# Kernel tuning notes

Hardware: AMD Instinct MI355X
Metric: run time of the kernel (lower is better)

The kernel has to match this reference:

```python
import jax, jax.numpy as jnp
import numpy as np
import math

B, R, C = 4, 512, 512
E, H, D, M, F = 256, 16, 16, 16, 512  # embed, heads, qkv_dim, ms_hidden, ff_hidden
EPS = 1e-5


def setup_inputs() -> dict:
    key = jax.random.key(0)
    ks = jax.random.split(key, 20)
    s = lambda fan_in: 1.0 / math.sqrt(fan_in)
    u = lambda k, shape, lim: jax.random.uniform(k, shape, jnp.float32, -lim, lim)
    mix1_init = (1 / 2) ** 0.5
    mix2_init = (1 / 16) ** 0.5
    return {
        "row_emb": jax.random.normal(ks[0], (B, R, E), jnp.float32),
        "col_emb": jax.random.normal(ks[1], (B, C, E), jnp.float32),
        "cost_mat": jax.random.uniform(ks[2], (B, R, C), jnp.float32),
        "Wq": u(ks[3], (E, H * D), s(E)),
        "Wk": u(ks[4], (E, H * D), s(E)),
        "Wv": u(ks[5], (E, H * D), s(E)),
        "mix1_w": u(ks[6], (H, 2, M), mix1_init),
        "mix1_b": u(ks[7], (H, M), mix1_init),
        "mix2_w": u(ks[8], (H, M, 1), mix2_init),
        "mix2_b": u(ks[9], (H, 1), mix2_init),
        "Wc": u(ks[10], (H * D, E), s(H * D)),
        "bc": u(ks[11], (E,), s(H * D)),
        "W1": u(ks[12], (E, F), s(E)),
        "b1": u(ks[13], (F,), s(E)),
        "W2": u(ks[14], (F, E), s(F)),
        "b2": u(ks[15], (E,), s(F)),
        "g1": jnp.ones((E,), jnp.float32),
        "be1": jnp.zeros((E,), jnp.float32),
        "g2": jnp.ones((E,), jnp.float32),
        "be2": jnp.zeros((E,), jnp.float32),
    }


def _instance_norm(x, gamma, beta):
    # InstanceNorm1d on x permuted to (B, E, L): normalize over seq dim per (b, channel)
    mean = jnp.mean(x, axis=1, keepdims=True)          # [B,1,E]
    var = jnp.mean((x - mean) ** 2, axis=1, keepdims=True)
    return (x - mean) * jax.lax.rsqrt(var + EPS) * gamma + beta


def reference(row_emb, col_emb, cost_mat, Wq, Wk, Wv, mix1_w, mix1_b, mix2_w,
              mix2_b, Wc, bc, W1, b1, W2, b2, g1, be1, g2, be2):
    # QKV projections, split heads: [B,L,H*D] -> [B,H,L,D]
    q = (row_emb @ Wq).reshape(B, R, H, D).transpose(0, 2, 1, 3)
    k = (col_emb @ Wk).reshape(B, C, H, D).transpose(0, 2, 1, 3)
    v = (col_emb @ Wv).reshape(B, C, H, D).transpose(0, 2, 1, 3)

    dot = jnp.einsum('bhrd,bhcd->bhrc', q, k) / math.sqrt(D)
    cost = jnp.broadcast_to(cost_mat[:, None, :, :], (B, H, R, C))
    two = jnp.stack((dot, cost), axis=-1)               # [B,H,R,C,2]

    # per-head 2 -> M -> 1 mixing MLP over scores
    ms1 = jnp.einsum('bhrcs,hsm->bhrcm', two, mix1_w) + mix1_b[None, :, None, None, :]
    ms1 = jax.nn.relu(ms1)
    mixed = jnp.einsum('bhrcm,hm->bhrc', ms1, mix2_w[:, :, 0]) + mix2_b[:, 0][None, :, None, None]

    weights = jax.nn.softmax(mixed, axis=-1)            # [B,H,R,C]
    out = jnp.einsum('bhrc,bhcd->bhrd', weights, v)
    out_concat = out.transpose(0, 2, 1, 3).reshape(B, R, H * D)

    mh = out_concat @ Wc + bc                           # multi_head_combine

    # TransformerFFN with instance norm
    x = _instance_norm(row_emb + mh, g1, be1)
    ffn = jax.nn.relu(x @ W1 + b1) @ W2 + b2
    return _instance_norm(x + ffn, g2, be2)
```

## Files before the change

kernel.cpp:

```cpp
#include <hip/hip_runtime.h>
#include <hip/hip_bf16.h>

typedef __hip_bfloat16 bf16;
typedef __hip_bfloat162 bf162;
typedef _Float16 f16;
typedef __attribute__((ext_vector_type(2))) _Float16 h2;
typedef __attribute__((ext_vector_type(4))) _Float16 f16x4;
typedef __attribute__((ext_vector_type(8))) short short8;
typedef __attribute__((ext_vector_type(4))) short short4v;
typedef __attribute__((ext_vector_type(4))) float f32x4;

#define B_ 4
#define R_ 512
#define C_ 512
#define E_ 256
#define H_ 16
#define D_ 16

__device__ __forceinline__ float b2f(bf16 x) { return __bfloat162float(x); }
__device__ __forceinline__ void stout(bf16* p, float v) { *p = __float2bfloat16(v); }
__device__ __forceinline__ void stout(f16* p, float v) { *p = (f16)v; }

__global__ __launch_bounds__(256) void transpose_cvt_kernel(
    const float* __restrict__ Wq, const float* __restrict__ Wk, const float* __restrict__ Wv,
    const float* __restrict__ Wc, const float* __restrict__ W1, const float* __restrict__ W2,
    bf16* __restrict__ WqT, bf16* __restrict__ WkT, bf16* __restrict__ WvT,
    bf16* __restrict__ WcT, bf16* __restrict__ W1T, bf16* __restrict__ W2T,
    float* __restrict__ statsZ)
{
    __shared__ bf16 tile[32][33];
    const int wsel = blockIdx.y;
    const int tx = blockIdx.x;
    if (wsel == 0 && tx >= 64) {
        const int idx = (tx - 64) * 256 + threadIdx.x;
        if (idx < 4096) statsZ[idx] = 0.f;
        return;
    }
    const float* src; bf16* dst; int K, N; float scl = 1.0f;
    switch (wsel) {
        case 0: src = Wq; dst = WqT; K = 256; N = 256; scl = 0.25f; break;
        case 1: src = Wk; dst = WkT; K = 256; N = 256; break;
        case 2: src = Wv; dst = WvT; K = 256; N = 256; break;
        case 3: src = Wc; dst = WcT; K = 256; N = 256; break;
        case 4: src = W1; dst = W1T; K = 256; N = 512; break;
        default: src = W2; dst = W2T; K = 512; N = 256; break;
    }
    const int ntiles = (K >> 5) * (N >> 5);
    if (tx >= ntiles) return;
    const int ncnt = N >> 5;
    const int tk = tx / ncnt, tn = tx % ncnt;
    const int c = threadIdx.x & 31, r = threadIdx.x >> 5;
#pragma unroll
    for (int i = 0; i < 4; i++)
        tile[r + i * 8][c] = __float2bfloat16(scl * src[(size_t)(tk * 32 + r + i * 8) * N + tn * 32 + c]);
    __syncthreads();
#pragma unroll
    for (int i = 0; i < 4; i++)
        dst[(size_t)(tn * 32 + r + i * 8) * K + tk * 32 + c] = tile[c][r + i * 8];
}

template <int AMODE, typename OT, int BM, int BN, bool BIAS, int RES, bool RELU, bool STATS>
__device__ __forceinline__ void mfma_gemm_body(
    const void* __restrict__ Ap, const bf16* __restrict__ BT,
    const float* __restrict__ bias, const void* __restrict__ Res,
    const float* __restrict__ normS, const float* __restrict__ normG, const float* __restrict__ normB,
    float* __restrict__ statsOut, OT* __restrict__ Cout,
    int M, int N, int K, int bx, int by)
{
    constexpr int MT = BM / 32, NT = BN / 32;
    constexpr int AEL = BM * 64 / 256, BEL = BN * 64 / 256;
    __shared__ __align__(16) bf16 As[BM * 80];
    __shared__ __align__(16) bf16 Bs[BN * 80];
    const int tid = threadIdx.x;
    const int wid = tid >> 6, lane = tid & 63;
    const int wm = wid >> 1, wn = wid & 1;
    const int fr = lane & 15, quad = lane >> 4;
    const int m0 = by * BM, n0 = bx * BN;
    const int arow = (AEL == 16) ? (tid >> 2) : (tid >> 3);
    const int akg  = (AEL == 16) ? ((tid & 3) << 4) : ((tid & 7) << 3);
    const int brow = (BEL == 16) ? (tid >> 2) : (tid >> 3);
    const int bkg  = (BEL == 16) ? ((tid & 3) << 4) : ((tid & 7) << 3);

    f32x4 acc[MT][NT];
#pragma unroll
    for (int mt = 0; mt < MT; mt++)
#pragma unroll
        for (int nt = 0; nt < NT; nt++) acc[mt][nt] = (f32x4){0.f, 0.f, 0.f, 0.f};

    for (int k0 = 0; k0 < K; k0 += 64) {
        if constexpr (AMODE == 0) {
            const short8* gp = (const short8*)((const bf16*)Ap + (size_t)(m0 + arow) * K + k0 + akg);
#pragma unroll
            for (int t8 = 0; t8 < AEL / 8; t8++) *(short8*)(&As[arow * 80 + akg + 8 * t8]) = gp[t8];
        } else if constexpr (AMODE == 1) {
            const float4* gp = (const float4*)((const float*)Ap + (size_t)(m0 + arow) * K + k0 + akg);
#pragma unroll
            for (int j = 0; j < AEL / 4; j++) {
                const float4 f = gp[j];
                *(bf162*)(&As[arow * 80 + akg + j * 4])     = __float22bfloat162_rn(make_float2(f.x, f.y));
                *(bf162*)(&As[arow * 80 + akg + j * 4 + 2]) = __float22bfloat162_rn(make_float2(f.z, f.w));
            }
        } else {
            const int bb = (m0 + arow) >> 9;
            const bf16* ap = (const bf16*)Ap + (size_t)(m0 + arow) * K + k0 + akg;
            bf16 tmp[AEL];
#pragma unroll
            for (int t8 = 0; t8 < AEL / 8; t8++) *(short8*)(tmp + 8 * t8) = ((const short8*)ap)[t8];
#pragma unroll
            for (int j = 0; j < AEL; j++) {
                const int e = k0 + akg + j;
                const float s = normS[bb * 256 + e], sq = normS[1024 + bb * 256 + e];
                const float mn = s * (1.f / 512.f);
                float var = sq * (1.f / 512.f) - mn * mn; var = fmaxf(var, 0.f);
                As[arow * 80 + akg + j] = __float2bfloat16(
                    (b2f(tmp[j]) - mn) * rsqrtf(var + 1e-5f) * normG[e] + normB[e]);
            }
        }
        {
            const short8* gp = (const short8*)(BT + (size_t)(n0 + brow) * K + k0 + bkg);
#pragma unroll
            for (int t8 = 0; t8 < BEL / 8; t8++) *(short8*)(&Bs[brow * 80 + bkg + 8 * t8]) = gp[t8];
        }
        __syncthreads();

        short8 af[MT][2], bfr[NT][2];
#pragma unroll
        for (int mt = 0; mt < MT; mt++) {
            const int ar = wm * (BM / 2) + mt * 16 + fr;
#pragma unroll
            for (int kh = 0; kh < 2; kh++)
                af[mt][kh] = *(const short8*)(&As[ar * 80 + quad * 8 + kh * 32]);
        }
#pragma unroll
        for (int nt = 0; nt < NT; nt++) {
            const int br = wn * (BN / 2) + nt * 16 + fr;
#pragma unroll
            for (int kh = 0; kh < 2; kh++)
                bfr[nt][kh] = *(const short8*)(&Bs[br * 80 + quad * 8 + kh * 32]);
        }
#pragma unroll
        for (int kh = 0; kh < 2; kh++)
#pragma unroll
            for (int mt = 0; mt < MT; mt++)
#pragma unroll
                for (int nt = 0; nt < NT; nt++)
                    acc[mt][nt] = __builtin_amdgcn_mfma_f32_16x16x32_bf16(
                        af[mt][kh], bfr[nt][kh], acc[mt][nt], 0, 0, 0);
        __syncthreads();
    }

    float vsum[NT], vss[NT];
#pragma unroll
    for (int nt = 0; nt < NT; nt++) { vsum[nt] = 0.f; vss[nt] = 0.f; }
#pragma unroll
    for (int mt = 0; mt < MT; mt++) {
#pragma unroll
        for (int nt = 0; nt < NT; nt++) {
#pragma unroll
            for (int i = 0; i < 4; i++) {
                const int row = m0 + wm * (BM / 2) + mt * 16 + quad * 4 + i;
                const int col = n0 + wn * (BN / 2) + nt * 16 + fr;
                float v = acc[mt][nt][i];
                if (BIAS) v += bias[col];
                if constexpr (RES == 1) v += ((const float*)Res)[(size_t)row * N + col];
                if constexpr (RES == 3) {
                    const int bb = row >> 9;
                    const float yv = b2f(((const bf16*)Res)[(size_t)row * N + col]);
                    const float s = normS[bb * 256 + col], sq = normS[1024 + bb * 256 + col];
                    const float mn = s * (1.f / 512.f);
                    float var = sq * (1.f / 512.f) - mn * mn; var = fmaxf(var, 0.f);
                    v += (yv - mn) * rsqrtf(var + 1e-5f) * normG[col] + normB[col];
                }
                if (RELU) v = fmaxf(v, 0.f);
                stout(&Cout[(size_t)row * N + col], v);
                if (STATS) { vsum[nt] += v; vss[nt] += v * v; }
            }
        }
    }
    if constexpr (STATS) {
        float* sred = (float*)As;
#pragma unroll
        for (int nt = 0; nt < NT; nt++) {
            float a = vsum[nt]; a += __shfl_xor(a, 16, 64); a += __shfl_xor(a, 32, 64);
            float c = vss[nt];  c += __shfl_xor(c, 16, 64); c += __shfl_xor(c, 32, 64);
            if (quad == 0) {
                const int cl = wn * (BN / 2) + nt * 16 + fr;
                sred[wm * (2 * BN) + cl * 2 + 0] = a;
                sred[wm * (2 * BN) + cl * 2 + 1] = c;
            }
        }
        __syncthreads();
        if (tid < 2 * BN) {
            const int cl = tid >> 1, w = tid & 1;
            const float tot = sred[cl * 2 + w] + sred[2 * BN + cl * 2 + w];
            atomicAdd(&statsOut[w * 1024 + (m0 >> 9) * 256 + n0 + cl], tot);
        }
    }
}

template <int AMODE, typename OT, int BM, int BN, bool BIAS, int RES, bool RELU, bool STATS>
__global__ __launch_bounds__(256) void mfma_gemm_kernel(
    const void* __restrict__ Ap, const bf16* __restrict__ BT,
    const float* __restrict__ bias, const void* __restrict__ Res,
    const float* __restrict__ normS, const float* __restrict__ normG, const float* __restrict__ normB,
    float* __restrict__ statsOut, OT* __restrict__ Cout, int M, int N, int K)
{
    mfma_gemm_body<AMODE, OT, BM, BN, BIAS, RES, RELU, STATS>(
        Ap, BT, bias, Res, normS, normG, normB, statsOut, Cout,
        M, N, K, blockIdx.x, blockIdx.y);
}

__global__ __launch_bounds__(256) void qkv_kernel(
    const float* __restrict__ rowE, const float* __restrict__ colE,
    const bf16* __restrict__ WqT, const bf16* __restrict__ WkT, const bf16* __restrict__ WvT,
    f16* __restrict__ qo, f16* __restrict__ ko, f16* __restrict__ vo)
{
    const int z = blockIdx.z;
    const float* A = (z == 0) ? rowE : colE;
    const bf16* BT = (z == 0) ? WqT : (z == 1) ? WkT : WvT;
    f16* out = (z == 0) ? qo : (z == 1) ? ko : vo;
    mfma_gemm_body<1, f16, 32, 64, false, 0, false, false>(
        A, BT, nullptr, nullptr, nullptr, nullptr, nullptr, nullptr, out,
        2048, 256, 256, blockIdx.x, blockIdx.y);
}

__global__ __launch_bounds__(256) void attn_kernel(
    const f16* __restrict__ q, const f16* __restrict__ k, const f16* __restrict__ v,
    const float* __restrict__ cost, const float* __restrict__ m1w, const float* __restrict__ m1b,
    const float* __restrict__ m2w, const float* __restrict__ m2b,
    bf16* __restrict__ sa)
{
    __shared__ __align__(16) short kbuf[512 * 16];
    __shared__ __align__(16) _Float16 vbufT[16 * 520];

    const int rt = blockIdx.x, h = blockIdx.y, b = blockIdx.z;
    const int tid = threadIdx.x, wid = tid >> 6, lane = tid & 63;
    const int quad = lane >> 4, fr = lane & 15;
    const int row_m = rt * 64 + wid * 16 + fr;

    const f16x4 qf = *(const f16x4*)(q + (size_t)(b * R_ + row_m) * 256 + h * 16 + (quad << 2));

    {
        const int lc0 = tid >> 1, dp = (tid & 1) * 8;
        const size_t gbase = (size_t)(b * C_) * 256 + h * 16 + dp;
#pragma unroll
        for (int it = 0; it < 4; it++) {
            const int lc = it * 128 + lc0;
            const size_t g = gbase + (size_t)lc * 256;
            *(short8*)(&kbuf[lc * 16 + (dp ^ ((lc & 1) << 3))]) = *(const short8*)(k + g);
            const short8 vv = *(const short8*)(v + g);
#pragma unroll
            for (int u = 0; u < 8; u++) vbufT[(dp + u) * 520 + lc] = ((const _Float16*)&vv)[u];
        }
    }

    h2 w1a2[8], w1b2[8], b1h[8], w2p[8];
#pragma unroll
    for (int i = 0; i < 8; i++) {
        h2 t;
        t.x = (f16)m1w[h * 32 + 2 * i];      t.y = (f16)m1w[h * 32 + 2 * i + 1];      w1a2[i] = t;
        t.x = (f16)m1w[h * 32 + 16 + 2 * i]; t.y = (f16)m1w[h * 32 + 17 + 2 * i];     w1b2[i] = t;
        t.x = (f16)m1b[h * 16 + 2 * i];      t.y = (f16)m1b[h * 16 + 2 * i + 1];      b1h[i] = t;
        t.x = (f16)m2w[h * 16 + 2 * i];      t.y = (f16)m2w[h * 16 + 2 * i + 1];      w2p[i] = t;
    }
    const float b2v = m2b[h];
    const h2 zero2 = (h2)(f16)0;

    const float* crow = cost + (size_t)(b * R_ + row_m) * C_;
    float4 cf[2][8];
#pragma unroll
    for (int t = 0; t < 8; t++) cf[0][t] = *(const float4*)(crow + t * 16 + (quad << 2));

    __syncthreads();

    f32x4 oaccT = (f32x4){0.f, 0.f, 0.f, 0.f};
    float lsum = 0.f, m_run = -3.0e30f;

#pragma unroll
    for (int cs = 0; cs < 4; cs++) {
        if (cs < 3) {
#pragma unroll
            for (int t = 0; t < 8; t++)
                cf[(cs + 1) & 1][t] = *(const float4*)(crow + (cs + 1) * 128 + t * 16 + (quad << 2));
        }
        f32x4 sc[8];
#pragma unroll
        for (int t = 0; t < 8; t++) {
            const int c = cs * 128 + t * 16 + fr;
            const f16x4 kf = *(const f16x4*)(&kbuf[c * 16 + ((quad << 2) ^ ((fr & 1) << 3))]);
            sc[t] = __builtin_amdgcn_mfma_f32_16x16x16f16(kf, qf, (f32x4){0.f, 0.f, 0.f, 0.f}, 0, 0, 0);
        }
#pragma unroll
        for (int t = 0; t < 8; t++) {
            const float4 cq = cf[cs & 1][t];
            const float carr[4] = {cq.x, cq.y, cq.z, cq.w};
#pragma unroll
            for (int i = 0; i < 4; i++) {
                const f16 doth = (f16)sc[t][i], csth = (f16)carr[i];
                h2 dot2; dot2.x = doth; dot2.y = doth;
                h2 cst2; cst2.x = csth; cst2.y = csth;
                h2 acc2 = zero2;
#pragma unroll
                for (int mm = 0; mm < 8; mm++) {
                    h2 tt = dot2 * w1a2[mm] + b1h[mm];
                    tt = cst2 * w1b2[mm] + tt;
                    tt = __builtin_elementwise_max(tt, zero2);
                    acc2 = tt * w2p[mm] + acc2;
                }
                sc[t][i] = b2v + (float)acc2.x + (float)acc2.y;
            }
        }
        float mx = fmaxf(fmaxf(sc[0][0], sc[0][1]), fmaxf(sc[0][2], sc[0][3]));
#pragma unroll
        for (int t = 1; t < 8; t++)
            mx = fmaxf(mx, fmaxf(fmaxf(sc[t][0], sc[t][1]), fmaxf(sc[t][2], sc[t][3])));
        mx = fmaxf(mx, __shfl_xor(mx, 16, 64));
        mx = fmaxf(mx, __shfl_xor(mx, 32, 64));
        const float mnew = fmaxf(m_run, mx);
        const float fac = __expf(m_run - mnew);
        m_run = mnew;
        lsum *= fac;
        oaccT[0] *= fac; oaccT[1] *= fac; oaccT[2] *= fac; oaccT[3] *= fac;

#pragma unroll
        for (int p = 0; p < 8; p++) {
            f16x4 pf;
#pragma unroll
            for (int j = 0; j < 4; j++) {
                const float e = __expf(sc[p][j] - m_run);
                lsum += e;
                pf[j] = (f16)e;
            }
            const f16x4 vf = *(const f16x4*)(&vbufT[fr * 520 + cs * 128 + p * 16 + (quad << 2)]);
            oaccT = __builtin_amdgcn_mfma_f32_16x16x16f16(vf, pf, oaccT, 0, 0, 0);
        }
    }

    lsum += __shfl_xor(lsum, 16, 64);
    lsum += __shfl_xor(lsum, 32, 64);
    const float inv = 1.f / lsum;
    short4v o;
#pragma unroll
    for (int i = 0; i < 4; i++) o[i] = __builtin_bit_cast(short, __float2bfloat16(oaccT[i] * inv));
    *(short4v*)((short*)sa + (size_t)(b * R_ + row_m) * 256 + h * 16 + (quad << 2)) = o;
}

__global__ __launch_bounds__(256) void apply_in2_kernel(
    const bf16* __restrict__ xin, const float* __restrict__ stats,
    const float* __restrict__ g, const float* __restrict__ be, float* __restrict__ outp)
{
    const int base = (blockIdx.x * 256 + threadIdx.x) * 4;
    const int b = base >> 17;
    const bf162* xp = (const bf162*)(xin + base);
    const float2 x0 = __bfloat1622float2(xp[0]), x1 = __bfloat1622float2(xp[1]);
    const float xv[4] = {x0.x, x0.y, x1.x, x1.y};
    float4 rr;
    float* rp = (float*)&rr;
#pragma unroll
    for (int j = 0; j < 4; j++) {
        const int e = (base & 255) + j;
        const float s = stats[b * 256 + e], sq = stats[1024 + b * 256 + e];
        const float mn = s * (1.f / 512.f);
        float var = sq * (1.f / 512.f) - mn * mn; var = fmaxf(var, 0.f);
        rp[j] = (xv[j] - mn) * rsqrtf(var + 1e-5f) * g[e] + be[e];
    }
    *(float4*)(outp + base) = rr;
}

extern "C" void kernel_launch(void* const* d_in, const int* in_sizes, int n_in,
                              void* d_out, int out_size, void* d_ws, size_t ws_size,
                              hipStream_t stream)
{
    (void)in_sizes; (void)n_in; (void)out_size; (void)ws_size;
    const float* row_emb = (const float*)d_in[0];
    const float* col_emb = (const float*)d_in[1];
    const float* cost    = (const float*)d_in[2];
    const float* Wq  = (const float*)d_in[3];
    const float* Wk  = (const float*)d_in[4];
    const float* Wv  = (const float*)d_in[5];
    const float* m1w = (const float*)d_in[6];
    const float* m1b = (const float*)d_in[7];
    const float* m2w = (const float*)d_in[8];
    const float* m2b = (const float*)d_in[9];
    const float* Wc  = (const float*)d_in[10];
    const float* bc  = (const float*)d_in[11];
    const float* W1  = (const float*)d_in[12];
    const float* b1  = (const float*)d_in[13];
    const float* W2  = (const float*)d_in[14];
    const float* b2  = (const float*)d_in[15];
    const float* g1  = (const float*)d_in[16];
    const float* be1 = (const float*)d_in[17];
    const float* g2  = (const float*)d_in[18];
    const float* be2 = (const float*)d_in[19];
    float* out = (float*)d_out;

    char* w = (char*)d_ws;
    const size_t MB = 1u << 20;
    f16*  sq  = (f16*)(w + 0 * MB);
    f16*  sk  = (f16*)(w + 1 * MB);
    f16*  sv  = (f16*)(w + 2 * MB);
    bf16* sa  = (bf16*)(w + 3 * MB);
    bf16* sy  = (bf16*)(w + 4 * MB);
    bf16* st  = (bf16*)(w + 5 * MB);
    bf16* shm = (bf16*)(w + 6 * MB);
    bf16* WqT = (bf16*)(w + 8 * MB);
    bf16* WkT = WqT + 65536;
    bf16* WvT = WkT + 65536;
    bf16* WcT = WvT + 65536;
    bf16* W1T = WcT + 65536;
    bf16* W2T = W1T + 131072;
    float* stats1 = (float*)(w + 9 * MB);
    float* stats2 = stats1 + 2048;

    const dim3 blk(256);

    transpose_cvt_kernel<<<dim3(128, 6), blk, 0, stream>>>(
        Wq, Wk, Wv, Wc, W1, W2, WqT, WkT, WvT, WcT, W1T, W2T, stats1);

    qkv_kernel<<<dim3(4, 64, 3), blk, 0, stream>>>(row_emb, col_emb, WqT, WkT, WvT, sq, sk, sv);

    attn_kernel<<<dim3(8, 16, 4), blk, 0, stream>>>(
        sq, sk, sv, cost, m1w, m1b, m2w, m2b, sa);

    mfma_gemm_kernel<0, bf16, 32, 32, true, 1, false, true><<<dim3(8, 64), blk, 0, stream>>>(
        sa, WcT, bc, row_emb, nullptr, nullptr, nullptr, stats1, sy, 2048, 256, 256);

    mfma_gemm_kernel<2, bf16, 32, 64, true, 0, true, false><<<dim3(8, 64), blk, 0, stream>>>(
        sy, W1T, b1, nullptr, stats1, g1, be1, nullptr, shm, 2048, 512, 256);

    mfma_gemm_kernel<0, bf16, 32, 32, true, 3, false, true><<<dim3(8, 64), blk, 0, stream>>>(
        shm, W2T, b2, sy, stats1, g1, be1, stats2, st, 2048, 256, 512);

    apply_in2_kernel<<<dim3(512), blk, 0, stream>>>(st, stats2, g2, be2, out);
}
```

Before: 153.2 us.

## Fuse weight conversion into QKV GEMM and enlarge GEMM M-tiles

Removes the separate transpose/convert launch. The QKV GEMM now reads fp32 Wq/Wk/Wv directly, applies the query scale, and writes them transposed into shared memory as bf16. The Wc/W1/W2 transposes and the stats zeroing run as extra blocks inside the same launch. The downstream GEMMs switch from BM=32 to BM=64 tiles with half the grid rows, to improve data reuse. The risk is that the three transposes in the same launch may not finish before later kernels need them; that is fine only because kernels on one stream run in order. The strided scalar LDS writes in the fused B load could cause bank conflicts, and the larger tiles leave fewer blocks to fill the CUs.

Result: no change. 156.2 us (+2.0%).

```diff
diff --git a/kernel.cpp b/kernel.cpp
--- a/kernel.cpp
+++ b/kernel.cpp
@@ -21,51 +21,13 @@
 __device__ __forceinline__ void stout(bf16* p, float v) { *p = __float2bfloat16(v); }
 __device__ __forceinline__ void stout(f16* p, float v) { *p = (f16)v; }
 
-__global__ __launch_bounds__(256) void transpose_cvt_kernel(
-    const float* __restrict__ Wq, const float* __restrict__ Wk, const float* __restrict__ Wv,
-    const float* __restrict__ Wc, const float* __restrict__ W1, const float* __restrict__ W2,
-    bf16* __restrict__ WqT, bf16* __restrict__ WkT, bf16* __restrict__ WvT,
-    bf16* __restrict__ WcT, bf16* __restrict__ W1T, bf16* __restrict__ W2T,
-    float* __restrict__ statsZ)
-{
-    __shared__ bf16 tile[32][33];
-    const int wsel = blockIdx.y;
-    const int tx = blockIdx.x;
-    if (wsel == 0 && tx >= 64) {
-        const int idx = (tx - 64) * 256 + threadIdx.x;
-        if (idx < 4096) statsZ[idx] = 0.f;
-        return;
-    }
-    const float* src; bf16* dst; int K, N; float scl = 1.0f;
-    switch (wsel) {
-        case 0: src = Wq; dst = WqT; K = 256; N = 256; scl = 0.25f; break;
-        case 1: src = Wk; dst = WkT; K = 256; N = 256; break;
-        case 2: src = Wv; dst = WvT; K = 256; N = 256; break;
-        case 3: src = Wc; dst = WcT; K = 256; N = 256; break;
-        case 4: src = W1; dst = W1T; K = 256; N = 512; break;
-        default: src = W2; dst = W2T; K = 512; N = 256; break;
-    }
-    const int ntiles = (K >> 5) * (N >> 5);
-    if (tx >= ntiles) return;
-    const int ncnt = N >> 5;
-    const int tk = tx / ncnt, tn = tx % ncnt;
-    const int c = threadIdx.x & 31, r = threadIdx.x >> 5;
-#pragma unroll
-    for (int i = 0; i < 4; i++)
-        tile[r + i * 8][c] = __float2bfloat16(scl * src[(size_t)(tk * 32 + r + i * 8) * N + tn * 32 + c]);
-    __syncthreads();
-#pragma unroll
-    for (int i = 0; i < 4; i++)
-        dst[(size_t)(tn * 32 + r + i * 8) * K + tk * 32 + c] = tile[c][r + i * 8];
-}
-
-template <int AMODE, typename OT, int BM, int BN, bool BIAS, int RES, bool RELU, bool STATS>
+template <int AMODE, typename OT, int BM, int BN, bool BIAS, int RES, bool RELU, bool STATS, int BSRC = 0>
 __device__ __forceinline__ void mfma_gemm_body(
     const void* __restrict__ Ap, const bf16* __restrict__ BT,
     const float* __restrict__ bias, const void* __restrict__ Res,
     const float* __restrict__ normS, const float* __restrict__ normG, const float* __restrict__ normB,
     float* __restrict__ statsOut, OT* __restrict__ Cout,
-    int M, int N, int K, int bx, int by)
+    int M, int N, int K, int bx, int by, float wscl = 1.0f)
 {
     constexpr int MT = BM / 32, NT = BN / 32;
     constexpr int AEL = BM * 64 / 256, BEL = BN * 64 / 256;
@@ -116,10 +78,23 @@
                     (b2f(tmp[j]) - mn) * rsqrtf(var + 1e-5f) * normG[e] + normB[e]);
             }
         }
-        {
+        if constexpr (BSRC == 0) {
             const short8* gp = (const short8*)(BT + (size_t)(n0 + brow) * K + k0 + bkg);
 #pragma unroll
             for (int t8 = 0; t8 < BEL / 8; t8++) *(short8*)(&Bs[brow * 80 + bkg + 8 * t8]) = gp[t8];
+        } else {
+            constexpr int NSEG = BN / 4;
+            const int kk = tid & 63;
+            const int ns = (tid >> 6) * NSEG;
+            const float* wp = (const float*)BT + (size_t)(k0 + kk) * N + n0 + ns;
+#pragma unroll
+            for (int j4 = 0; j4 < NSEG / 4; j4++) {
+                const float4 f = *(const float4*)(wp + 4 * j4);
+                Bs[(ns + 4 * j4 + 0) * 80 + kk] = __float2bfloat16(wscl * f.x);
+                Bs[(ns + 4 * j4 + 1) * 80 + kk] = __float2bfloat16(wscl * f.y);
+                Bs[(ns + 4 * j4 + 2) * 80 + kk] = __float2bfloat16(wscl * f.z);
+                Bs[(ns + 4 * j4 + 3) * 80 + kk] = __float2bfloat16(wscl * f.w);
+            }
         }
         __syncthreads();
 
@@ -210,18 +185,52 @@
         M, N, K, blockIdx.x, blockIdx.y);
 }
 
-__global__ __launch_bounds__(256) void qkv_kernel(
+__global__ __launch_bounds__(256) void prep_qkv_kernel(
     const float* __restrict__ rowE, const float* __restrict__ colE,
-    const bf16* __restrict__ WqT, const bf16* __restrict__ WkT, const bf16* __restrict__ WvT,
+    const float* __restrict__ Wq, const float* __restrict__ Wk, const float* __restrict__ Wv,
+    const float* __restrict__ Wc, const float* __restrict__ W1, const float* __restrict__ W2,
+    bf16* __restrict__ WcT, bf16* __restrict__ W1T, bf16* __restrict__ W2T,
+    float* __restrict__ statsZ,
     f16* __restrict__ qo, f16* __restrict__ ko, f16* __restrict__ vo)
 {
-    const int z = blockIdx.z;
+    const int bid = blockIdx.x;
+    const int tid = threadIdx.x;
+
+    if (bid >= 384) {
+        const int spare = bid - 384;
+        if (spare >= 320) {
+            statsZ[(spare - 320) * 256 + tid] = 0.f;
+            return;
+        }
+        __shared__ bf16 tile[32][33];
+        const float* src; bf16* dst; int K, N, tix;
+        if (spare < 64)       { src = Wc; dst = WcT; K = 256; N = 256; tix = spare; }
+        else if (spare < 192) { src = W1; dst = W1T; K = 256; N = 512; tix = spare - 64; }
+        else                  { src = W2; dst = W2T; K = 512; N = 256; tix = spare - 192; }
+        const int ncnt = N >> 5;
+        const int tk = tix / ncnt, tn = tix % ncnt;
+        const int c = tid & 31, r = tid >> 5;
+#pragma unroll
+        for (int i = 0; i < 4; i++)
+            tile[r + i * 8][c] = __float2bfloat16(src[(size_t)(tk * 32 + r + i * 8) * N + tn * 32 + c]);
+        __syncthreads();
+#pragma unroll
+        for (int i = 0; i < 4; i++)
+            dst[(size_t)(tn * 32 + r + i * 8) * K + tk * 32 + c] = tile[c][r + i * 8];
+        return;
+    }
+
+    const int z = bid >> 7;
+    const int rem = bid & 127;
+    const int bx = rem & 3, by = rem >> 2;
     const float* A = (z == 0) ? rowE : colE;
-    const bf16* BT = (z == 0) ? WqT : (z == 1) ? WkT : WvT;
+    const float* W = (z == 0) ? Wq : (z == 1) ? Wk : Wv;
     f16* out = (z == 0) ? qo : (z == 1) ? ko : vo;
-    mfma_gemm_body<1, f16, 32, 64, false, 0, false, false>(
-        A, BT, nullptr, nullptr, nullptr, nullptr, nullptr, nullptr, out,
-        2048, 256, 256, blockIdx.x, blockIdx.y);
+    const float scl = (z == 0) ? 0.25f : 1.0f;
+
+    mfma_gemm_body<1, f16, 64, 64, false, 0, false, false, 1>(
+        A, (const bf16*)W, nullptr, nullptr, nullptr, nullptr, nullptr, nullptr, out,
+        2048, 256, 256, bx, by, scl);
 }
 
 __global__ __launch_bounds__(256) void attn_kernel(
@@ -403,10 +412,7 @@
     bf16* sy  = (bf16*)(w + 4 * MB);
     bf16* st  = (bf16*)(w + 5 * MB);
     bf16* shm = (bf16*)(w + 6 * MB);
-    bf16* WqT = (bf16*)(w + 8 * MB);
-    bf16* WkT = WqT + 65536;
-    bf16* WvT = WkT + 65536;
-    bf16* WcT = WvT + 65536;
+    bf16* WcT = (bf16*)(w + 8 * MB);
     bf16* W1T = WcT + 65536;
     bf16* W2T = W1T + 131072;
     float* stats1 = (float*)(w + 9 * MB);
@@ -414,21 +420,20 @@
 
     const dim3 blk(256);
 
-    transpose_cvt_kernel<<<dim3(128, 6), blk, 0, stream>>>(
-        Wq, Wk, Wv, Wc, W1, W2, WqT, WkT, WvT, WcT, W1T, W2T, stats1);
-
-    qkv_kernel<<<dim3(4, 64, 3), blk, 0, stream>>>(row_emb, col_emb, WqT, WkT, WvT, sq, sk, sv);
+    prep_qkv_kernel<<<dim3(720), blk, 0, stream>>>(
+        row_emb, col_emb, Wq, Wk, Wv, Wc, W1, W2,
+        WcT, W1T, W2T, stats1, sq, sk, sv);
 
     attn_kernel<<<dim3(8, 16, 4), blk, 0, stream>>>(
         sq, sk, sv, cost, m1w, m1b, m2w, m2b, sa);
 
-    mfma_gemm_kernel<0, bf16, 32, 32, true, 1, false, true><<<dim3(8, 64), blk, 0, stream>>>(
+    mfma_gemm_kernel<0, bf16, 64, 32, true, 1, false, true><<<dim3(8, 32), blk, 0, stream>>>(
         sa, WcT, bc, row_emb, nullptr, nullptr, nullptr, stats1, sy, 2048, 256, 256);
 
-    mfma_gemm_kernel<2, bf16, 32, 64, true, 0, true, false><<<dim3(8, 64), blk, 0, stream>>>(
+    mfma_gemm_kernel<2, bf16, 64, 64, true, 0, true, false><<<dim3(8, 32), blk, 0, stream>>>(
         sy, W1T, b1, nullptr, stats1, g1, be1, nullptr, shm, 2048, 512, 256);
 
-    mfma_gemm_kernel<0, bf16, 32, 32, true, 3, false, true><<<dim3(8, 64), blk, 0, stream>>>(
+    mfma_gemm_kernel<0, bf16, 64, 32, true, 3, false, true><<<dim3(8, 32), blk, 0, stream>>>(
         shm, W2T, b2, sy, stats1, g1, be1, stats2, st, 2048, 256, 512);
 
     apply_in2_kernel<<<dim3(512), blk, 0, stream>>>(st, stats2, g2, be2, out);
```
